# Kernel tuning notes

Hardware: AMD Instinct MI355X
Metric: run time of the kernel (lower is better)

The kernel has to match this reference:

```python
import jax, jax.numpy as jnp
import numpy as np

N_NODES = 100000
N_EDGES = 1600000
IN, HID, OUT = 256, 128, 1


def setup_inputs() -> dict:
    key = jax.random.key(0)
    ks = jax.random.split(key, 12)
    inp = {
        "x": jax.random.normal(ks[0], (N_NODES, IN), dtype=jnp.float32),
        "W_t": jax.random.normal(ks[1], (IN, HID), dtype=jnp.float32) / np.sqrt(IN),
        "b_t": jnp.zeros((HID,), dtype=jnp.float32),
        "W_self0": jax.random.normal(ks[2], (HID, HID), dtype=jnp.float32) / np.sqrt(HID),
        "b_self0": jnp.zeros((HID,), dtype=jnp.float32),
        "W_neigh0": jax.random.normal(ks[3], (HID, HID), dtype=jnp.float32) / np.sqrt(HID),
        "W_self1": jax.random.normal(ks[4], (HID, HID), dtype=jnp.float32) / np.sqrt(HID),
        "b_self1": jnp.zeros((HID,), dtype=jnp.float32),
        "W_neigh1": jax.random.normal(ks[5], (HID, HID), dtype=jnp.float32) / np.sqrt(HID),
        "W_fin": jax.random.normal(ks[6], (HID, OUT), dtype=jnp.float32) / np.sqrt(HID),
        "src": jax.random.randint(ks[7], (N_EDGES,), 0, N_NODES, dtype=jnp.int64 if jax.config.jax_enable_x64 else jnp.int32),
        "dst": jax.random.randint(ks[8], (N_EDGES,), 0, N_NODES, dtype=jnp.int64 if jax.config.jax_enable_x64 else jnp.int32),
    }
    return inp


def _sage_mean_layer(h, src, dst, W_self, b_self, W_neigh):
    # DGL SAGEConv('mean'): fc_self(h_dst) + fc_neigh(mean over in-neighbors)
    msg = h[src]  # [E, H] gather
    summed = jax.ops.segment_sum(msg, dst, num_segments=N_NODES)
    deg = jax.ops.segment_sum(jnp.ones((msg.shape[0],), h.dtype), dst, num_segments=N_NODES)
    h_neigh = summed / jnp.maximum(deg, 1.0)[:, None]
    out = h @ W_self + b_self + h_neigh @ W_neigh
    return jax.nn.relu(out)  # dropout is identity in eval mode


def reference(x, W_t, b_t, W_self0, b_self0, W_neigh0, W_self1, b_self1, W_neigh1, W_fin, src, dst):
    h = x @ W_t + b_t
    h = _sage_mean_layer(h, src, dst, W_self0, b_self0, W_neigh0)
    h = _sage_mean_layer(h, src, dst, W_self1, b_self1, W_neigh1)
    out = h @ W_fin  # [N, 1]
    return out.squeeze()
```

## Files before the change

kernel.cpp:

```cpp
#include <hip/hip_runtime.h>
#include <hip/hip_fp16.h>

#define HIDDEN 128
#define BSHIFT 9
#define NBUCK_MAX 256

using f32x4 = __attribute__((ext_vector_type(4))) float;
using f16x8 = __attribute__((ext_vector_type(8))) _Float16;

__device__ __forceinline__ void gload16(const void* g, void* l) {
    __builtin_amdgcn_global_load_lds((const __attribute__((address_space(1))) void*)g,
                                     (__attribute__((address_space(3))) void*)l,
                                     16, 0, 0);
}

__global__ void zero_ints(int* __restrict__ a, int n) {
    int i = blockIdx.x * 256 + threadIdx.x;
    if (i < n) a[i] = 0;
}

__launch_bounds__(256)
__global__ void bucket_hist(const int* __restrict__ dst, int* __restrict__ bcnt, int e) {
    __shared__ int c[NBUCK_MAX];
    const int t = threadIdx.x;
    c[t] = 0;
    __syncthreads();
    const int tile0 = blockIdx.x * 4096;
    const int end = min(e, tile0 + 4096);
    for (int i = tile0 + t; i < end; i += 256)
        atomicAdd(&c[dst[i] >> BSHIFT], 1);
    __syncthreads();
    if (c[t]) atomicAdd(&bcnt[t], c[t]);
}

__global__ void scan_buckets(const int* __restrict__ bcnt, int* __restrict__ boffs,
                             int* __restrict__ cursor, int nb) {
    __shared__ int sd[256];
    const int t = threadIdx.x;
    int v = (t < nb) ? bcnt[t] : 0;
    sd[t] = v;
    __syncthreads();
    for (int o = 1; o < 256; o <<= 1) {
        int add = (t >= o) ? sd[t - o] : 0;
        __syncthreads();
        sd[t] += add;
        __syncthreads();
    }
    const int ex = sd[t] - v;
    if (t < nb) { boffs[t] = ex; cursor[t] = ex; }
    if (t == nb - 1) boffs[nb] = ex + v;
}

__launch_bounds__(256)
__global__ void partition_pairs(const int* __restrict__ src, const int* __restrict__ dst,
                                int* __restrict__ cursor,
                                unsigned long long* __restrict__ pairs, int e) {
    __shared__ int cnt[NBUCK_MAX];
    __shared__ int base[NBUCK_MAX];
    const int t = threadIdx.x;
    const int tile0 = blockIdx.x * 4096;
    cnt[t] = 0;
    __syncthreads();
    int s[16], d[16], b[16];
    #pragma unroll
    for (int j = 0; j < 16; ++j) {
        const int i = tile0 + j * 256 + t;
        if (i < e) {
            d[j] = dst[i];
            s[j] = src[i];
            b[j] = d[j] >> BSHIFT;
            atomicAdd(&cnt[b[j]], 1);
        } else {
            b[j] = -1;
        }
    }
    __syncthreads();
    const int c = cnt[t];
    base[t] = c ? atomicAdd(&cursor[t], c) : 0;
    __syncthreads();
    cnt[t] = 0;
    __syncthreads();
    #pragma unroll
    for (int j = 0; j < 16; ++j) {
        if (b[j] >= 0) {
            const int r = atomicAdd(&cnt[b[j]], 1);
            pairs[(size_t)base[b[j]] + r] =
                ((unsigned long long)(unsigned)d[j] << 32) | (unsigned)s[j];
        }
    }
}

__launch_bounds__(256)
__global__ void place_csr2(const unsigned long long* __restrict__ pairs,
                           const int* __restrict__ boffs,
                           int* __restrict__ offs, int* __restrict__ csr,
                           int n, int e) {
    __shared__ int cnt[1 << BSHIFT];
    __shared__ int sc[256];
    const int b = blockIdx.x;
    const int t = threadIdx.x;
    const int node0 = b << BSHIFT;
    const int nn = min(1 << BSHIFT, n - node0);
    cnt[t] = 0;
    cnt[t + 256] = 0;
    __syncthreads();
    const int beg = boffs[b], end = boffs[b + 1];
    for (int i = beg + t; i < end; i += 256)
        atomicAdd(&cnt[(int)(pairs[i] >> 32) - node0], 1);
    __syncthreads();
    const int a0 = cnt[2 * t], a1 = cnt[2 * t + 1];
    const int s = a0 + a1;
    sc[t] = s;
    __syncthreads();
    for (int o = 1; o < 256; o <<= 1) {
        int add = (t >= o) ? sc[t - o] : 0;
        __syncthreads();
        sc[t] += add;
        __syncthreads();
    }
    const int g0 = beg + sc[t] - s;
    const int g1 = g0 + a0;
    if (2 * t < nn)     offs[node0 + 2 * t] = g0;
    if (2 * t + 1 < nn) offs[node0 + 2 * t + 1] = g1;
    __syncthreads();
    cnt[2 * t] = g0;
    cnt[2 * t + 1] = g1;
    if (node0 + nn == n && t == 0) offs[n] = e;
    __syncthreads();
    for (int i = beg + t; i < end; i += 256) {
        const unsigned long long pr = pairs[i];
        const int dd = (int)(pr >> 32) - node0;
        const int ss = (int)(unsigned)pr;
        const int p = atomicAdd(&cnt[dd], 1);
        csr[p] = ss;
    }
}

__global__ void pack_weights(const float* __restrict__ W_t, const float* __restrict__ Ws0,
                             const float* __restrict__ Wn0, const float* __restrict__ Ws1,
                             const float* __restrict__ Wn1,
                             __half* p_t, __half* p_l0, __half* p_l1) {
    const int bid = blockIdx.x;
    const float* W; __half* out; int b0; int S0;
    if (bid < 16)      { W = W_t; out = p_t;  b0 = 0;  S0 = 0; }
    else if (bid < 24) { W = Ws0; out = p_l0; b0 = 16; S0 = 0; }
    else if (bid < 32) { W = Wn0; out = p_l0; b0 = 24; S0 = 4; }
    else if (bid < 40) { W = Ws1; out = p_l1; b0 = 32; S0 = 0; }
    else               { W = Wn1; out = p_l1; b0 = 40; S0 = 4; }
    const int idx = (bid - b0) * 256 + threadIdx.x;
    const int step = idx >> 9;
    const int r = idx & 511;
    const int l = r & 63;
    const int col = (r >> 6) * 16 + (l & 15);
    const int k0 = step * 32 + ((l >> 4) << 3);
    const size_t o = (size_t)(S0 + step) * 4096 + (size_t)r * 8;
    #pragma unroll
    for (int j = 0; j < 8; ++j) {
        float f = W[(k0 + j) * HIDDEN + col];
        __half h = __float2half_rn(f);
        out[o + j] = h;
        out[32768 + o + j] = __float2half_rn((f - __half2float(h)) * 32.0f);
    }
}

template <bool RELU, bool FINAL>
__launch_bounds__(256, 8)
__global__ void gemm32(const __half* __restrict__ A0, const __half* __restrict__ A1,
                       const __half* __restrict__ Wp,
                       const float* __restrict__ bias,
                       const float* __restrict__ wfin,
                       void* __restrict__ outv, int nrows) {
    __shared__ __align__(16) __half As[8][2][64][8];
    __shared__ float red[FINAL ? 32 : 1][4];

    const int t = threadIdx.x;
    const int lane = t & 63;
    const int w = t >> 6;
    const int blockRow0 = blockIdx.x * 32;

    {
        const int koff = (lane >> 4) << 3;
        #pragma unroll
        for (int i = 0; i < 2; ++i) {
            const int step = w * 2 + i;
            const __half* Abase = (step < 4) ? A0 : A1;
            const int kk = (step & 3) * 32 + koff;
            #pragma unroll
            for (int rt = 0; rt < 2; ++rt) {
                const int row = min(blockRow0 + rt * 16 + (lane & 15), nrows - 1);
                gload16(Abase + (size_t)row * HIDDEN + kk, &As[step][rt][0][0]);
            }
        }
    }
    __syncthreads();

    f32x4 acc[2][2];
    #pragma unroll
    for (int i = 0; i < 2; ++i)
        #pragma unroll
        for (int j = 0; j < 2; ++j) acc[i][j] = (f32x4){0.f, 0.f, 0.f, 0.f};

    const _Float16 S = (_Float16)0.03125f;

    #pragma unroll
    for (int step = 0; step < 8; ++step) {
        const __half* wb = Wp + (size_t)step * 4096 + (w * 2) * 512 + lane * 8;
        f16x8 a[2], asr[2];
        #pragma unroll
        for (int rt = 0; rt < 2; ++rt) {
            a[rt] = *(const f16x8*)&As[step][rt][lane][0];
            asr[rt] = a[rt] * S;
        }
        #pragma unroll
        for (int c2 = 0; c2 < 2; ++c2) {
            f16x8 wh = *(const f16x8*)(wb + c2 * 512);
            f16x8 wl = *(const f16x8*)(wb + 32768 + c2 * 512);
            acc[0][c2] = __builtin_amdgcn_mfma_f32_16x16x32_f16(a[0], wh, acc[0][c2], 0, 0, 0);
            acc[1][c2] = __builtin_amdgcn_mfma_f32_16x16x32_f16(a[1], wh, acc[1][c2], 0, 0, 0);
            acc[0][c2] = __builtin_amdgcn_mfma_f32_16x16x32_f16(asr[0], wl, acc[0][c2], 0, 0, 0);
            acc[1][c2] = __builtin_amdgcn_mfma_f32_16x16x32_f16(asr[1], wl, acc[1][c2], 0, 0, 0);
        }
    }

    if constexpr (FINAL) {
        float part[2][4];
        #pragma unroll
        for (int rt = 0; rt < 2; ++rt)
            #pragma unroll
            for (int j = 0; j < 4; ++j) part[rt][j] = 0.f;
        #pragma unroll
        for (int c2 = 0; c2 < 2; ++c2) {
            const int col = w * 32 + c2 * 16 + (lane & 15);
            const float wf = wfin[col];
            const float bc = bias[col];
            #pragma unroll
            for (int rt = 0; rt < 2; ++rt)
                #pragma unroll
                for (int j = 0; j < 4; ++j) {
                    float v = acc[rt][c2][j] + bc;
                    if (RELU) v = fmaxf(v, 0.f);
                    part[rt][j] = fmaf(v, wf, part[rt][j]);
                }
        }
        #pragma unroll
        for (int o = 1; o < 16; o <<= 1)
            #pragma unroll
            for (int rt = 0; rt < 2; ++rt)
                #pragma unroll
                for (int j = 0; j < 4; ++j)
                    part[rt][j] += __shfl_xor(part[rt][j], o, 64);
        if ((lane & 15) == 0) {
            #pragma unroll
            for (int rt = 0; rt < 2; ++rt)
                #pragma unroll
                for (int j = 0; j < 4; ++j)
                    red[rt * 16 + ((lane >> 4) << 2) + j][w] = part[rt][j];
        }
        __syncthreads();
        if (t < 32) {
            const int r = blockRow0 + t;
            if (r < nrows)
                ((float*)outv)[r] = red[t][0] + red[t][1] + red[t][2] + red[t][3];
        }
    } else {
        __half* out = (__half*)outv;
        #pragma unroll
        for (int c2 = 0; c2 < 2; ++c2) {
            const int col = w * 32 + c2 * 16 + (lane & 15);
            const float bc = bias[col];
            #pragma unroll
            for (int rt = 0; rt < 2; ++rt) {
                const int r0 = blockRow0 + rt * 16 + ((lane >> 4) << 2);
                #pragma unroll
                for (int j = 0; j < 4; ++j) {
                    const int r = r0 + j;
                    if (r < nrows) {
                        float v = acc[rt][c2][j] + bc;
                        if (RELU) v = fmaxf(v, 0.f);
                        out[(size_t)r * HIDDEN + col] = __float2half(v);
                    }
                }
            }
        }
    }
}

__launch_bounds__(256, 8)
__global__ void gemm_x16v(const float* __restrict__ X, const __half* __restrict__ Wp,
                          const float* __restrict__ bias,
                          __half* __restrict__ outp, int nrows) {
    __shared__ __align__(16) float Xs[8][2][64][4];

    const int t = threadIdx.x;
    const int lane = t & 63;
    const int w = t >> 6;
    const int blockRow0 = blockIdx.x * 16;

    {
        const int row = min(blockRow0 + (lane & 15), nrows - 1);
        const int kg = (lane >> 4) << 3;
        #pragma unroll
        for (int i = 0; i < 2; ++i) {
            const int step = w * 2 + i;
            #pragma unroll
            for (int hf = 0; hf < 2; ++hf) {
                const float* src = X + (size_t)row * 256 + step * 32 + kg + hf * 4;
                gload16(src, &Xs[step][hf][0][0]);
            }
        }
    }
    __syncthreads();

    f32x4 acc[2];
    acc[0] = (f32x4){0.f, 0.f, 0.f, 0.f};
    acc[1] = (f32x4){0.f, 0.f, 0.f, 0.f};

    const _Float16 S = (_Float16)0.03125f;

    #pragma unroll
    for (int step = 0; step < 8; ++step) {
        const __half* wb = Wp + (size_t)step * 4096 + (w * 2) * 512 + lane * 8;
        f32x4 x0 = *(const f32x4*)&Xs[step][0][lane][0];
        f32x4 x1 = *(const f32x4*)&Xs[step][1][lane][0];
        f16x8 a;
        #pragma unroll
        for (int j = 0; j < 4; ++j) a[j] = (_Float16)x0[j];
        #pragma unroll
        for (int j = 0; j < 4; ++j) a[4 + j] = (_Float16)x1[j];
        f16x8 asr = a * S;
        #pragma unroll
        for (int c2 = 0; c2 < 2; ++c2) {
            f16x8 wh = *(const f16x8*)(wb + c2 * 512);
            f16x8 wl = *(const f16x8*)(wb + 32768 + c2 * 512);
            acc[c2] = __builtin_amdgcn_mfma_f32_16x16x32_f16(a, wh, acc[c2], 0, 0, 0);
            acc[c2] = __builtin_amdgcn_mfma_f32_16x16x32_f16(asr, wl, acc[c2], 0, 0, 0);
        }
    }

    #pragma unroll
    for (int c2 = 0; c2 < 2; ++c2) {
        const int col = w * 32 + c2 * 16 + (lane & 15);
        const float bc = bias[col];
        const int r0 = blockRow0 + ((lane >> 4) << 2);
        #pragma unroll
        for (int j = 0; j < 4; ++j) {
            const int r = r0 + j;
            if (r < nrows)
                outp[(size_t)r * HIDDEN + col] = __float2half(acc[c2][j] + bc);
        }
    }
}

__global__ void aggregate_h16(const __half* __restrict__ h, const int* __restrict__ offs,
                              const int* __restrict__ csr,
                              __half* __restrict__ agg, int n) {
    const int node = blockIdx.x * 4 + (threadIdx.x >> 6);
    if (node >= n) return;
    const int lane = threadIdx.x & 63;
    const int slot = lane >> 4;
    const int c8 = (lane & 15) * 8;
    const int start = offs[node];
    const int d = offs[node + 1] - start;
    float a[8] = {0.f, 0.f, 0.f, 0.f, 0.f, 0.f, 0.f, 0.f};
    for (int i = slot; i < d; i += 16) {
        #pragma unroll
        for (int u = 0; u < 4; ++u) {
            const int e = i + u * 4;
            if (e < d) {
                const int s = csr[start + e];
                uint4 raw = *(const uint4*)&h[(size_t)s * HIDDEN + c8];
                const __half2* hp = (const __half2*)&raw;
                #pragma unroll
                for (int m = 0; m < 4; ++m) {
                    float2 f = __half22float2(hp[m]);
                    a[2 * m] += f.x;
                    a[2 * m + 1] += f.y;
                }
            }
        }
    }
    #pragma unroll
    for (int k = 0; k < 8; ++k) {
        a[k] += __shfl_xor(a[k], 16, 64);
        a[k] += __shfl_xor(a[k], 32, 64);
    }
    if (slot == 0) {
        const float inv = 1.0f / (float)max(d, 1);
        uint4 raw;
        __half2* op = (__half2*)&raw;
        #pragma unroll
        for (int m = 0; m < 4; ++m)
            op[m] = __floats2half2_rn(a[2 * m] * inv, a[2 * m + 1] * inv);
        *(uint4*)&agg[(size_t)node * HIDDEN + c8] = raw;
    }
}

extern "C" void kernel_launch(void* const* d_in, const int* in_sizes, int n_in,
                              void* d_out, int out_size, void* d_ws, size_t ws_size,
                              hipStream_t stream) {
    const float* x     = (const float*)d_in[0];
    const float* W_t   = (const float*)d_in[1];
    const float* b_t   = (const float*)d_in[2];
    const float* W_s0  = (const float*)d_in[3];
    const float* b_s0  = (const float*)d_in[4];
    const float* W_n0  = (const float*)d_in[5];
    const float* W_s1  = (const float*)d_in[6];
    const float* b_s1  = (const float*)d_in[7];
    const float* W_n1  = (const float*)d_in[8];
    const float* W_fin = (const float*)d_in[9];
    const int*   src   = (const int*)d_in[10];
    const int*   dst   = (const int*)d_in[11];
    float* out = (float*)d_out;

    const int N = in_sizes[0] / 256;
    const int E = in_sizes[10];

    size_t off_b = 0;
    auto carve = [&](size_t bytes) {
        size_t cur = off_b;
        off_b = (off_b + bytes + 255) & ~(size_t)255;
        return cur;
    };
    char* base = (char*)d_ws;
    int* offs   = (int*)(base + carve((size_t)(N + 1) * 4));
    int* bcnt   = (int*)(base + carve(NBUCK_MAX * 4));
    int* boffs  = (int*)(base + carve((NBUCK_MAX + 1) * 4));
    int* cursor = (int*)(base + carve(NBUCK_MAX * 4));
    int* csr    = (int*)(base + carve((size_t)E * 4));
    unsigned long long* pairs = (unsigned long long*)(base + carve((size_t)E * 8));
    __half* wp_t  = (__half*)(base + carve((size_t)65536 * 2));
    __half* wp_l0 = (__half*)(base + carve((size_t)65536 * 2));
    __half* wp_l1 = (__half*)(base + carve((size_t)65536 * 2));
    __half* hA  = (__half*)(base + carve((size_t)N * HIDDEN * 2));
    __half* hB  = (__half*)(base + carve((size_t)N * HIDDEN * 2));
    __half* agp = (__half*)(base + carve((size_t)N * HIDDEN * 2));
    (void)ws_size; (void)n_in; (void)out_size;

    const int nBuck = (N + (1 << BSHIFT) - 1) >> BSHIFT;

    hipLaunchKernelGGL(zero_ints, dim3(1), dim3(256), 0, stream, bcnt, NBUCK_MAX);
    hipLaunchKernelGGL(bucket_hist, dim3((E + 4095) / 4096), dim3(256), 0, stream, dst, bcnt, E);
    hipLaunchKernelGGL(scan_buckets, dim3(1), dim3(256), 0, stream, bcnt, boffs, cursor, nBuck);
    hipLaunchKernelGGL(partition_pairs, dim3((E + 4095) / 4096), dim3(256), 0, stream,
                       src, dst, cursor, pairs, E);
    hipLaunchKernelGGL(place_csr2, dim3(nBuck), dim3(256), 0, stream, pairs, boffs, offs, csr, N, E);

    hipLaunchKernelGGL(pack_weights, dim3(48), dim3(256), 0, stream,
                       W_t, W_s0, W_n0, W_s1, W_n1, wp_t, wp_l0, wp_l1);

    const int g32 = (N + 31) / 32;
    const int g16 = (N + 15) / 16;
    const int nodeGrid = (N + 3) / 4;

    hipLaunchKernelGGL(gemm_x16v, dim3(g16), dim3(256), 0, stream,
                       x, wp_t, b_t, hA, N);
    hipLaunchKernelGGL(aggregate_h16, dim3(nodeGrid), dim3(256), 0, stream, hA, offs, csr, agp, N);
    hipLaunchKernelGGL((gemm32<true, false>), dim3(g32), dim3(256), 0, stream,
                       hA, agp, wp_l0, b_s0, (const float*)nullptr, (void*)hB, N);
    hipLaunchKernelGGL(aggregate_h16, dim3(nodeGrid), dim3(256), 0, stream, hB, offs, csr, agp, N);
    hipLaunchKernelGGL((gemm32<true, true>), dim3(g32), dim3(256), 0, stream,
                       hB, agp, wp_l1, b_s1, W_fin, (void*)out, N);
}
```

Measured before the change: 292.1 us.

## Fuse neighbor-mean aggregation into SAGE layer GEMM and widen input GEMM tile

Neighbor-mean aggregation now runs inside the layer GEMM kernel. Each wave gathers and averages 8 nodes' neighbors directly into the LDS A-tile, so the separate aggregate kernels and the fp16 agg buffer round trip are removed. The input projection GEMM moves from 16 to 32 rows per block so each weight fragment load is reused across two row tiles, with launch bounds lowered to 4 blocks. The risk is that the irregular gather, now serialized inside GEMM blocks, gets less latency hiding and occupancy than the standalone aggregate kernel had.

Measured after the change: 277.3 us. -5.1%, faster.

```diff
diff --git a/kernel.cpp b/kernel.cpp
--- a/kernel.cpp
+++ b/kernel.cpp
@@ -165,7 +165,8 @@
 
 template <bool RELU, bool FINAL>
 __launch_bounds__(256, 8)
-__global__ void gemm32(const __half* __restrict__ A0, const __half* __restrict__ A1,
+__global__ void sage32(const __half* __restrict__ h,
+                       const int* __restrict__ offs, const int* __restrict__ csr,
                        const __half* __restrict__ Wp,
                        const float* __restrict__ bias,
                        const float* __restrict__ wfin,
@@ -179,16 +180,52 @@
     const int blockRow0 = blockIdx.x * 32;
 
     {
-        const int koff = (lane >> 4) << 3;
-        #pragma unroll
-        for (int i = 0; i < 2; ++i) {
-            const int step = w * 2 + i;
-            const __half* Abase = (step < 4) ? A0 : A1;
-            const int kk = (step & 3) * 32 + koff;
-            #pragma unroll
-            for (int rt = 0; rt < 2; ++rt) {
-                const int row = min(blockRow0 + rt * 16 + (lane & 15), nrows - 1);
-                gload16(Abase + (size_t)row * HIDDEN + kk, &As[step][rt][0][0]);
+        const int kk = w * 32 + ((lane >> 4) << 3);
+        #pragma unroll
+        for (int rt = 0; rt < 2; ++rt) {
+            const int row = min(blockRow0 + rt * 16 + (lane & 15), nrows - 1);
+            gload16(h + (size_t)row * HIDDEN + kk, &As[w][rt][0][0]);
+        }
+    }
+
+    {
+        const int slot = lane >> 4;
+        const int c8 = (lane & 15) * 8;
+        #pragma unroll 1
+        for (int nd = 0; nd < 8; ++nd) {
+            const int rl = w * 8 + nd;
+            const int node = min(blockRow0 + rl, nrows - 1);
+            const int start = offs[node];
+            const int d = offs[node + 1] - start;
+            float a[8] = {0.f, 0.f, 0.f, 0.f, 0.f, 0.f, 0.f, 0.f};
+            for (int i = slot; i < d; i += 16) {
+                #pragma unroll
+                for (int u = 0; u < 4; ++u) {
+                    const int e = i + u * 4;
+                    if (e < d) {
+                        const int s = csr[start + e];
+                        uint4 raw = *(const uint4*)&h[(size_t)s * HIDDEN + c8];
+                        const __half2* hp = (const __half2*)&raw;
+                        #pragma unroll
+                        for (int m = 0; m < 4; ++m) {
+                            float2 f = __half22float2(hp[m]);
+                            a[2 * m] += f.x;
+                            a[2 * m + 1] += f.y;
+                        }
+                    }
+                }
+            }
+            #pragma unroll
+            for (int k = 0; k < 8; ++k) {
+                a[k] += __shfl_xor(a[k], 16, 64);
+                a[k] += __shfl_xor(a[k], 32, 64);
+            }
+            if (slot == 0) {
+                const float inv = 1.0f / (float)max(d, 1);
+                f16x8 v;
+                #pragma unroll
+                for (int j = 0; j < 8; ++j) v[j] = (_Float16)(a[j] * inv);
+                *(f16x8*)&As[4 + (lane >> 2)][rl >> 4][(rl & 15) + 16 * (lane & 3)][0] = v;
             }
         }
     }
@@ -285,113 +322,82 @@
     }
 }
 
-__launch_bounds__(256, 8)
-__global__ void gemm_x16v(const float* __restrict__ X, const __half* __restrict__ Wp,
+__launch_bounds__(256, 4)
+__global__ void gemm_x32v(const float* __restrict__ X, const __half* __restrict__ Wp,
                           const float* __restrict__ bias,
                           __half* __restrict__ outp, int nrows) {
-    __shared__ __align__(16) float Xs[8][2][64][4];
+    __shared__ __align__(16) float Xs[8][2][2][64][4];
 
     const int t = threadIdx.x;
     const int lane = t & 63;
     const int w = t >> 6;
-    const int blockRow0 = blockIdx.x * 16;
+    const int blockRow0 = blockIdx.x * 32;
 
     {
-        const int row = min(blockRow0 + (lane & 15), nrows - 1);
-        const int kg = (lane >> 4) << 3;
-        #pragma unroll
-        for (int i = 0; i < 2; ++i) {
-            const int step = w * 2 + i;
-            #pragma unroll
-            for (int hf = 0; hf < 2; ++hf) {
-                const float* src = X + (size_t)row * 256 + step * 32 + kg + hf * 4;
-                gload16(src, &Xs[step][hf][0][0]);
-            }
-        }
-    }
-    __syncthreads();
-
-    f32x4 acc[2];
-    acc[0] = (f32x4){0.f, 0.f, 0.f, 0.f};
-    acc[1] = (f32x4){0.f, 0.f, 0.f, 0.f};
+        const int rt = w >> 1, hf = w & 1;
+        const int row = min(blockRow0 + rt * 16 + (lane & 15), nrows - 1);
+        const int k0 = ((lane >> 4) << 3) + hf * 4;
+        #pragma unroll
+        for (int step = 0; step < 8; ++step) {
+            const float* src = X + (size_t)row * 256 + step * 32 + k0;
+            gload16(src, &Xs[step][rt][hf][0][0]);
+        }
+    }
+    __syncthreads();
+
+    f32x4 acc[2][2];
+    #pragma unroll
+    for (int i = 0; i < 2; ++i)
+        #pragma unroll
+        for (int j = 0; j < 2; ++j) acc[i][j] = (f32x4){0.f, 0.f, 0.f, 0.f};
 
     const _Float16 S = (_Float16)0.03125f;
 
     #pragma unroll
     for (int step = 0; step < 8; ++step) {
         const __half* wb = Wp + (size_t)step * 4096 + (w * 2) * 512 + lane * 8;
-        f32x4 x0 = *(const f32x4*)&Xs[step][0][lane][0];
-        f32x4 x1 = *(const f32x4*)&Xs[step][1][lane][0];
-        f16x8 a;
-        #pragma unroll
-        for (int j = 0; j < 4; ++j) a[j] = (_Float16)x0[j];
-        #pragma unroll
-        for (int j = 0; j < 4; ++j) a[4 + j] = (_Float16)x1[j];
-        f16x8 asr = a * S;
+        f16x8 wh[2], wl[2];
         #pragma unroll
         for (int c2 = 0; c2 < 2; ++c2) {
-            f16x8 wh = *(const f16x8*)(wb + c2 * 512);
-            f16x8 wl = *(const f16x8*)(wb + 32768 + c2 * 512);
-            acc[c2] = __builtin_amdgcn_mfma_f32_16x16x32_f16(a, wh, acc[c2], 0, 0, 0);
-            acc[c2] = __builtin_amdgcn_mfma_f32_16x16x32_f16(asr, wl, acc[c2], 0, 0, 0);
-        }
+            wh[c2] = *(const f16x8*)(wb + c2 * 512);
+            wl[c2] = *(const f16x8*)(wb + 32768 + c2 * 512);
+        }
+        f16x8 a[2], asr[2];
+        #pragma unroll
+        for (int r2 = 0; r2 < 2; ++r2) {
+            f32x4 x0 = *(const f32x4*)&Xs[step][r2][0][lane][0];
+            f32x4 x1 = *(const f32x4*)&Xs[step][r2][1][lane][0];
+            f16x8 hh;
+            #pragma unroll
+            for (int j = 0; j < 4; ++j) hh[j] = (_Float16)x0[j];
+            #pragma unroll
+            for (int j = 0; j < 4; ++j) hh[4 + j] = (_Float16)x1[j];
+            a[r2] = hh;
+            asr[r2] = hh * S;
+        }
+        #pragma unroll
+        for (int r2 = 0; r2 < 2; ++r2)
+            #pragma unroll
+            for (int c2 = 0; c2 < 2; ++c2) {
+                acc[r2][c2] = __builtin_amdgcn_mfma_f32_16x16x32_f16(a[r2], wh[c2], acc[r2][c2], 0, 0, 0);
+                acc[r2][c2] = __builtin_amdgcn_mfma_f32_16x16x32_f16(asr[r2], wl[c2], acc[r2][c2], 0, 0, 0);
+            }
     }
 
     #pragma unroll
     for (int c2 = 0; c2 < 2; ++c2) {
         const int col = w * 32 + c2 * 16 + (lane & 15);
         const float bc = bias[col];
-        const int r0 = blockRow0 + ((lane >> 4) << 2);
-        #pragma unroll
-        for (int j = 0; j < 4; ++j) {
-            const int r = r0 + j;
-            if (r < nrows)
-                outp[(size_t)r * HIDDEN + col] = __float2half(acc[c2][j] + bc);
-        }
-    }
-}
-
-__global__ void aggregate_h16(const __half* __restrict__ h, const int* __restrict__ offs,
-                              const int* __restrict__ csr,
-                              __half* __restrict__ agg, int n) {
-    const int node = blockIdx.x * 4 + (threadIdx.x >> 6);
-    if (node >= n) return;
-    const int lane = threadIdx.x & 63;
-    const int slot = lane >> 4;
-    const int c8 = (lane & 15) * 8;
-    const int start = offs[node];
-    const int d = offs[node + 1] - start;
-    float a[8] = {0.f, 0.f, 0.f, 0.f, 0.f, 0.f, 0.f, 0.f};
-    for (int i = slot; i < d; i += 16) {
-        #pragma unroll
-        for (int u = 0; u < 4; ++u) {
-            const int e = i + u * 4;
-            if (e < d) {
-                const int s = csr[start + e];
-                uint4 raw = *(const uint4*)&h[(size_t)s * HIDDEN + c8];
-                const __half2* hp = (const __half2*)&raw;
-                #pragma unroll
-                for (int m = 0; m < 4; ++m) {
-                    float2 f = __half22float2(hp[m]);
-                    a[2 * m] += f.x;
-                    a[2 * m + 1] += f.y;
-                }
-            }
-        }
-    }
-    #pragma unroll
-    for (int k = 0; k < 8; ++k) {
-        a[k] += __shfl_xor(a[k], 16, 64);
-        a[k] += __shfl_xor(a[k], 32, 64);
-    }
-    if (slot == 0) {
-        const float inv = 1.0f / (float)max(d, 1);
-        uint4 raw;
-        __half2* op = (__half2*)&raw;
-        #pragma unroll
-        for (int m = 0; m < 4; ++m)
-            op[m] = __floats2half2_rn(a[2 * m] * inv, a[2 * m + 1] * inv);
-        *(uint4*)&agg[(size_t)node * HIDDEN + c8] = raw;
+        #pragma unroll
+        for (int r2 = 0; r2 < 2; ++r2) {
+            const int r0 = blockRow0 + r2 * 16 + ((lane >> 4) << 2);
+            #pragma unroll
+            for (int j = 0; j < 4; ++j) {
+                const int r = r0 + j;
+                if (r < nrows)
+                    outp[(size_t)r * HIDDEN + col] = __float2half(acc[r2][c2][j] + bc);
+            }
+        }
     }
 }
 
@@ -433,7 +439,6 @@
     __half* wp_l1 = (__half*)(base + carve((size_t)65536 * 2));
     __half* hA  = (__half*)(base + carve((size_t)N * HIDDEN * 2));
     __half* hB  = (__half*)(base + carve((size_t)N * HIDDEN * 2));
-    __half* agp = (__half*)(base + carve((size_t)N * HIDDEN * 2));
     (void)ws_size; (void)n_in; (void)out_size;
 
     const int nBuck = (N + (1 << BSHIFT) - 1) >> BSHIFT;
@@ -449,15 +454,11 @@
                        W_t, W_s0, W_n0, W_s1, W_n1, wp_t, wp_l0, wp_l1);
 
     const int g32 = (N + 31) / 32;
-    const int g16 = (N + 15) / 16;
-    const int nodeGrid = (N + 3) / 4;
-
-    hipLaunchKernelGGL(gemm_x16v, dim3(g16), dim3(256), 0, stream,
+
+    hipLaunchKernelGGL(gemm_x32v, dim3(g32), dim3(256), 0, stream,
                        x, wp_t, b_t, hA, N);
-    hipLaunchKernelGGL(aggregate_h16, dim3(nodeGrid), dim3(256), 0, stream, hA, offs, csr, agp, N);
-    hipLaunchKernelGGL((gemm32<true, false>), dim3(g32), dim3(256), 0, stream,
-                       hA, agp, wp_l0, b_s0, (const float*)nullptr, (void*)hB, N);
-    hipLaunchKernelGGL(aggregate_h16, dim3(nodeGrid), dim3(256), 0, stream, hB, offs, csr, agp, N);
-    hipLaunchKernelGGL((gemm32<true, true>), dim3(g32), dim3(256), 0, stream,
-                       hB, agp, wp_l1, b_s1, W_fin, (void*)out, N);
-}
+    hipLaunchKernelGGL((sage32<true, false>), dim3(g32), dim3(256), 0, stream,
+                       hA, offs, csr, wp_l0, b_s0, (const float*)nullptr, (void*)hB, N);
+    hipLaunchKernelGGL((sage32<true, true>), dim3(g32), dim3(256), 0, stream,
+                       hB, offs, csr, wp_l1, b_s1, W_fin, (void*)out, N);
+}
```
